# Kernel tuning notes

Measured on AMD Instinct MI355X. Metric: run time of the kernel, lower is better.

The kernel has to match this reference:

```python
import jax, jax.numpy as jnp
import numpy as np

B, T, C, H = 2, 1024, 1024, 16
HD = C // H  # head_dim = 64


def setup_inputs() -> dict:
    key = jax.random.key(0)
    ks = jax.random.split(key, 11)
    s = 0.02  # init scale for weights
    inp = {
        "Q": jax.random.normal(ks[0], (B, T, C), jnp.float32),
        "K": jax.random.normal(ks[1], (B, T, C), jnp.float32),
        "V": jax.random.normal(ks[2], (B, T, C), jnp.float32),
        "Wq": jax.random.normal(ks[3], (C, C), jnp.float32) * s,
        "bq": jnp.zeros((C,), jnp.float32),
        "Wk": jax.random.normal(ks[4], (C, C), jnp.float32) * s,
        "bk": jnp.zeros((C,), jnp.float32),
        "Wv": jax.random.normal(ks[5], (C, C), jnp.float32) * s,
        "bv": jnp.zeros((C,), jnp.float32),
        "Wp": jax.random.normal(ks[6], (C, C), jnp.float32) * s,
        "bp": jax.random.normal(ks[7], (C,), jnp.float32) * s,
        # causal attention mask: True = masked (matches masked_fill semantics)
        "attn_mask": jnp.triu(jnp.ones((T, T), jnp.bool_), k=1),
    }
    return inp


def reference(Q, K, V, Wq, bq, Wk, bk, Wv, bv, Wp, bp, attn_mask):
    b, t, c = Q.shape

    def proj(x, W, bias):
        # nn.Linear: x @ W.T + b, then split heads -> [B, H, T, HD]
        return (x @ W.T + bias).reshape(b, t, H, HD).transpose(0, 2, 1, 3)

    q = proj(Q, Wq, bq)
    k = proj(K, Wk, bk)
    v = proj(V, Wv, bv)
    # scoreF: scaled dot-product -> [B, H, T, T]
    a = jnp.einsum('bhtd,bhsd->bhts', q, k) / jnp.sqrt(jnp.asarray(HD, q.dtype))
    a = jnp.where(attn_mask, -jnp.inf, a)  # masked_fill(attn_mask, -inf)
    a = jax.nn.softmax(a, axis=-1)  # ADropout is identity (p=0)
    y = jnp.einsum('bhts,bhsd->bhtd', a, v)  # a @ v
    y = y.transpose(0, 2, 1, 3).reshape(b, t, c)
    y = y @ Wp.T + bp  # P projection; RDropout identity (p=0)
    return (y, a)
```

## Files before the change

kernel.cpp:

```cpp
#include <hip/hip_runtime.h>
#include <hip/hip_bf16.h>

typedef short bf16x8 __attribute__((ext_vector_type(8)));
typedef float f32x4 __attribute__((ext_vector_type(4)));
typedef unsigned short u16;
typedef u16 u16x8 __attribute__((ext_vector_type(8)));

#define MFMA16(a, b, c) __builtin_amdgcn_mfma_f32_16x16x32_bf16(a, b, c, 0, 0, 0)


__device__ __forceinline__ u16 f2bf(float f) {
    unsigned u = __builtin_bit_cast(unsigned, f);
    unsigned r = (u + 0x7FFFu + ((u >> 16) & 1u)) >> 16;
    return (u16)r;
}

__global__ __launch_bounds__(256) void cvt_bf16(
    const float* __restrict__ Q, const float* __restrict__ K, const float* __restrict__ V,
    const float* __restrict__ Wq, const float* __restrict__ Wk, const float* __restrict__ Wv,
    const float* __restrict__ Wp,
    u16* __restrict__ Qb, u16* __restrict__ Kb, u16* __restrict__ Vb,
    u16* __restrict__ Wqb, u16* __restrict__ Wkb, u16* __restrict__ Wvb,
    u16* __restrict__ Wpb) {
    const int z = blockIdx.y;
    const float* src;
    u16* dst;
    int n;
    switch (z) {
        case 0: src = Q;  dst = Qb;  n = 1 << 21; break;
        case 1: src = K;  dst = Kb;  n = 1 << 21; break;
        case 2: src = V;  dst = Vb;  n = 1 << 21; break;
        case 3: src = Wq; dst = Wqb; n = 1 << 20; break;
        case 4: src = Wk; dst = Wkb; n = 1 << 20; break;
        case 5: src = Wv; dst = Wvb; n = 1 << 20; break;
        default: src = Wp; dst = Wpb; n = 1 << 20; break;
    }
    const int i = (blockIdx.x * 256 + threadIdx.x) * 8;
    if (i >= n) return;
    float4 f0 = *(const float4*)(src + i);
    float4 f1 = *(const float4*)(src + i + 4);
    u16x8 t;
    t[0] = f2bf(f0.x); t[1] = f2bf(f0.y); t[2] = f2bf(f0.z); t[3] = f2bf(f0.w);
    t[4] = f2bf(f1.x); t[5] = f2bf(f1.y); t[6] = f2bf(f1.z); t[7] = f2bf(f1.w);
    *(u16x8*)(dst + i) = t;
}

template <bool OF32>
__device__ inline void gemm_body(const u16* __restrict__ A,
                                 const u16* __restrict__ W,
                                 const float* __restrict__ bias,
                                 void* __restrict__ outp, int mode) {
    __shared__ u16 As[8 * 128 * 8];
    __shared__ u16 Bs[8 * 64 * 8];

    const int tid = threadIdx.x;
    const int wave = tid >> 6, lane = tid & 63;
    const int quad = lane >> 4, l16 = lane & 15;
    const int wm = (wave >> 1) * 64;
    const int wn = (wave & 1) * 32;
    const int m0 = blockIdx.y * 128;
    const int n0 = blockIdx.x * 64;

    f32x4 acc[4][2] = {};

    const int srow = tid >> 3;
    const int sseg = tid & 7;

    for (int kt = 0; kt < 16; ++kt) {
        const int k0 = kt * 64;
        __syncthreads();
#pragma unroll
        for (int rr = 0; rr < 4; ++rr) {
            int row = srow + rr * 32;
            *(uint4*)(As + ((sseg * 128 + row) * 8)) =
                *(const uint4*)(A + (size_t)(m0 + row) * 1024 + k0 + sseg * 8);
        }
#pragma unroll
        for (int rr = 0; rr < 2; ++rr) {
            int row = srow + rr * 32;
            *(uint4*)(Bs + ((sseg * 64 + row) * 8)) =
                *(const uint4*)(W + (size_t)(n0 + row) * 1024 + k0 + sseg * 8);
        }
        __syncthreads();
#pragma unroll
        for (int ks = 0; ks < 2; ++ks) {
            bf16x8 af[4], bfr[2];
#pragma unroll
            for (int mi = 0; mi < 4; ++mi)
                af[mi] = *(const bf16x8*)(As + (((ks * 4 + quad) * 128) + wm + mi * 16 + l16) * 8);
#pragma unroll
            for (int ni = 0; ni < 2; ++ni)
                bfr[ni] = *(const bf16x8*)(Bs + (((ks * 4 + quad) * 64) + wn + ni * 16 + l16) * 8);
#pragma unroll
            for (int mi = 0; mi < 4; ++mi)
#pragma unroll
                for (int ni = 0; ni < 2; ++ni)
                    acc[mi][ni] = MFMA16(af[mi], bfr[ni], acc[mi][ni]);
        }
    }

#pragma unroll
    for (int ni = 0; ni < 2; ++ni) {
        const int n = n0 + wn + ni * 16 + l16;
        const float bv = bias[n];
#pragma unroll
        for (int mi = 0; mi < 4; ++mi) {
#pragma unroll
            for (int r = 0; r < 4; ++r) {
                const int m = m0 + wm + mi * 16 + quad * 4 + r;
                const float val = acc[mi][ni][r] + bv;
                size_t idx;
                if (mode == 0) {
                    int b = m >> 10, t = m & 1023, h = n >> 6, d = n & 63;
                    idx = ((size_t)((b * 16 + h) * 1024 + t)) * 64 + d;
                } else if (mode == 1) {
                    int b = m >> 10, t = m & 1023, h = n >> 6, d = n & 63;
                    idx = ((size_t)((b * 16 + h) * 64 + d)) * 1024 + t;
                } else {
                    idx = (size_t)m * 1024 + n;
                }
                if (OF32) ((float*)outp)[idx] = val;
                else      ((u16*)outp)[idx] = f2bf(val);
            }
        }
    }
}

__global__ __launch_bounds__(256) void proj_qkv(
    const u16* __restrict__ Qb, const u16* __restrict__ Kb, const u16* __restrict__ Vb,
    const u16* __restrict__ Wqb, const u16* __restrict__ Wkb, const u16* __restrict__ Wvb,
    const float* __restrict__ bq, const float* __restrict__ bk, const float* __restrict__ bv,
    u16* __restrict__ q_ws, u16* __restrict__ k_ws, u16* __restrict__ vt_ws) {
    const int z = blockIdx.z;
    const u16* A = (z == 0) ? Qb : (z == 1) ? Kb : Vb;
    const u16* W = (z == 0) ? Wqb : (z == 1) ? Wkb : Wvb;
    const float* bias = (z == 0) ? bq : (z == 1) ? bk : bv;
    u16* out = (z == 0) ? q_ws : (z == 1) ? k_ws : vt_ws;
    gemm_body<false>(A, W, bias, out, (z == 2) ? 1 : 0);
}

__global__ __launch_bounds__(256) void proj_out(
    const u16* __restrict__ A, const u16* __restrict__ Wpb,
    const float* __restrict__ bp, float* __restrict__ y) {
    gemm_body<true>(A, Wpb, bp, y, 2);
}

__global__ __launch_bounds__(256) void attn_fused(
    const u16* __restrict__ q_ws, const u16* __restrict__ k_ws,
    const u16* __restrict__ vt_ws, float* __restrict__ a_out,
    u16* __restrict__ ao_ws) {
    __shared__ u16 P[4][1024];
    __shared__ float Ls[4][16];
    __shared__ float Osum[4][1024];

    const int tid = threadIdx.x;
    const int wave = tid >> 6, lane = tid & 63;
    const int quad = lane >> 4, l16 = lane & 15;
    const int strip = 63 - blockIdx.x;
    const int h = blockIdx.y, b = blockIdx.z;
    const int bh = b * 16 + h;
    const int wrow = strip * 16;
    const int nt = (strip >> 2) + 1;

    const u16* qh = q_ws + (size_t)bh * 65536;
    const u16* kh = k_ws + (size_t)bh * 65536;
    const u16* vh = vt_ws + (size_t)bh * 65536;
    float* ah = a_out + ((size_t)bh << 20);

    bf16x8 qf[2];
    qf[0] = *(const bf16x8*)(qh + (size_t)(wrow + l16) * 64 + quad * 8);
    qf[1] = *(const bf16x8*)(qh + (size_t)(wrow + l16) * 64 + 32 + quad * 8);

    f32x4 c[4][4] = {};
    float sum_r[4] = {0.f, 0.f, 0.f, 0.f};

#pragma unroll
    for (int s = 0; s < 4; ++s) {
        const int ct = wave + s * 4;
        if (ct < nt) {
#pragma unroll
            for (int ks = 0; ks < 2; ++ks)
#pragma unroll
                for (int cb = 0; cb < 4; ++cb) {
                    bf16x8 kf = *(const bf16x8*)(kh + (size_t)(ct * 64 + cb * 16 + l16) * 64 + ks * 32 + quad * 8);
                    c[s][cb] = MFMA16(qf[ks], kf, c[s][cb]);
                }
#pragma unroll
            for (int cb = 0; cb < 4; ++cb) {
                const int col = ct * 64 + cb * 16 + l16;
#pragma unroll
                for (int r = 0; r < 4; ++r) {
                    const int trow = wrow + quad * 4 + r;
                    float E = __expf(c[s][cb][r] * 0.125f - 20.0f);
                    if (col > trow) E = 0.0f;
                    c[s][cb][r] = E;
                    sum_r[r] += E;
                }
            }
        }
    }

    {
        const float4 zz = make_float4(0.f, 0.f, 0.f, 0.f);
        for (int ct = nt + wave; ct < 16; ct += 4) {
#pragma unroll
            for (int j = 0; j < 4; ++j)
                *(float4*)(ah + (size_t)(wrow + j * 4 + quad) * 1024 + ct * 64 + l16 * 4) = zz;
        }
    }

#pragma unroll
    for (int r = 0; r < 4; ++r) {
#pragma unroll
        for (int off = 1; off < 16; off <<= 1)
            sum_r[r] += __shfl_xor(sum_r[r], off);
    }
    if (l16 == 0) {
#pragma unroll
        for (int r = 0; r < 4; ++r) Ls[wave][quad * 4 + r] = sum_r[r];
    }
    __syncthreads();

    float rl[4];
#pragma unroll
    for (int r = 0; r < 4; ++r) {
        const int m = quad * 4 + r;
        rl[r] = 1.0f / (Ls[0][m] + Ls[1][m] + Ls[2][m] + Ls[3][m]);
    }

    f32x4 o[4] = {};
#pragma unroll
    for (int s = 0; s < 4; ++s) {
        const int ct = wave + s * 4;
        if (ct < nt) {
#pragma unroll
            for (int cb = 0; cb < 4; ++cb) {
                const int s_col = cb * 16 + l16;
                const int col = ct * 64 + s_col;
#pragma unroll
                for (int r = 0; r < 4; ++r) {
                    const int m = quad * 4 + r;
                    const float v = c[s][cb][r] * rl[r];
                    ah[(size_t)(wrow + m) * 1024 + col] = v;
                    P[wave][(s_col >> 3) * 128 + m * 8 + (s_col & 7)] = f2bf(v);
                }
            }
#pragma unroll
            for (int ks = 0; ks < 2; ++ks) {
                bf16x8 pf = *(const bf16x8*)(&P[wave][(ks * 4 + quad) * 128 + l16 * 8]);
#pragma unroll
                for (int nb = 0; nb < 4; ++nb) {
                    bf16x8 vf = *(const bf16x8*)(vh + (size_t)(nb * 16 + l16) * 1024 + ct * 64 + ks * 32 + quad * 8);
                    o[nb] = MFMA16(pf, vf, o[nb]);
                }
            }
        }
    }

#pragma unroll
    for (int nb = 0; nb < 4; ++nb)
#pragma unroll
        for (int r = 0; r < 4; ++r) {
            const int row = quad * 4 + r;
            const int d = nb * 16 + l16;
            Osum[wave][row * 64 + (d ^ ((row >> 2) << 4))] = o[nb][r];
        }
    __syncthreads();

#pragma unroll
    for (int i = 0; i < 4; ++i) {
        const int e = tid + i * 256;
        const int row = e >> 6, d = e & 63;
        const int sd = row * 64 + (d ^ ((row >> 2) << 4));
        const float v = Osum[0][sd] + Osum[1][sd] + Osum[2][sd] + Osum[3][sd];
        ao_ws[((size_t)(b * 1024 + wrow + row)) * 1024 + h * 64 + d] = f2bf(v);
    }
}

extern "C" void kernel_launch(void* const* d_in, const int* in_sizes, int n_in,
                              void* d_out, int out_size, void* d_ws, size_t ws_size,
                              hipStream_t stream) {
    const float* Q  = (const float*)d_in[0];
    const float* K  = (const float*)d_in[1];
    const float* V  = (const float*)d_in[2];
    const float* Wq = (const float*)d_in[3];
    const float* bq = (const float*)d_in[4];
    const float* Wk = (const float*)d_in[5];
    const float* bk = (const float*)d_in[6];
    const float* Wv = (const float*)d_in[7];
    const float* bv = (const float*)d_in[8];
    const float* Wp = (const float*)d_in[9];
    const float* bp = (const float*)d_in[10];

    float* y = (float*)d_out;
    float* a = y + (size_t)2 * 1024 * 1024;

    const size_t M1 = (size_t)1 << 20;
    u16* q_ws  = (u16*)d_ws;
    u16* k_ws  = q_ws  + 2 * M1;
    u16* vt_ws = k_ws  + 2 * M1;
    u16* ao_ws = vt_ws + 2 * M1;
    u16* Qb    = ao_ws + 2 * M1;
    u16* Kb    = Qb    + 2 * M1;
    u16* Vb    = Kb    + 2 * M1;
    u16* Wqb   = Vb    + 2 * M1;
    u16* Wkb   = Wqb   + M1;
    u16* Wvb   = Wkb   + M1;
    u16* Wpb   = Wvb   + M1;

    hipLaunchKernelGGL(cvt_bf16, dim3(1024, 7), dim3(256), 0, stream,
                       Q, K, V, Wq, Wk, Wv, Wp, Qb, Kb, Vb, Wqb, Wkb, Wvb, Wpb);
    hipLaunchKernelGGL(proj_qkv, dim3(16, 16, 3), dim3(256), 0, stream,
                       Qb, Kb, Vb, Wqb, Wkb, Wvb, bq, bk, bv, q_ws, k_ws, vt_ws);
    hipLaunchKernelGGL(attn_fused, dim3(64, 16, 2), dim3(256), 0, stream,
                       q_ws, k_ws, vt_ws, a, ao_ws);
    hipLaunchKernelGGL(proj_out, dim3(16, 16, 1), dim3(256), 0, stream,
                       ao_ws, Wpb, bp, y);
}
```

Baseline: 298.4 us.

## Use direct global-to-LDS loads in GEMMs and smaller M tile for output projection

The projection GEMM tile loads now use the global_load_lds builtin, which writes straight into shared memory without passing through registers. The shared-memory tile becomes row-major with 64-element rows instead of the previous k-segment-major layout. The GEMM is templated on the M tile size, and the output projection runs with a 64-row tile on a doubled grid to put more blocks on the GPU. The row-major LDS layout may cause bank conflicts on the MFMA fragment reads, and the GEMMs are small relative to the attention kernel.

```diff
diff --git a/kernel.cpp b/kernel.cpp
--- a/kernel.cpp
+++ b/kernel.cpp
@@ -45,54 +45,58 @@
     *(u16x8*)(dst + i) = t;
 }
 
-template <bool OF32>
+template <int BM, bool OF32>
 __device__ inline void gemm_body(const u16* __restrict__ A,
                                  const u16* __restrict__ W,
                                  const float* __restrict__ bias,
                                  void* __restrict__ outp, int mode) {
-    __shared__ u16 As[8 * 128 * 8];
-    __shared__ u16 Bs[8 * 64 * 8];
+    __shared__ u16 As[BM * 64];
+    __shared__ u16 Bs[64 * 64];
 
     const int tid = threadIdx.x;
     const int wave = tid >> 6, lane = tid & 63;
     const int quad = lane >> 4, l16 = lane & 15;
-    const int wm = (wave >> 1) * 64;
+    constexpr int WM = BM / 2;
+    constexpr int MI = WM / 16;
+    const int wm = (wave >> 1) * WM;
     const int wn = (wave & 1) * 32;
-    const int m0 = blockIdx.y * 128;
+    const int m0 = blockIdx.y * BM;
     const int n0 = blockIdx.x * 64;
 
-    f32x4 acc[4][2] = {};
-
-    const int srow = tid >> 3;
-    const int sseg = tid & 7;
+    f32x4 acc[MI][2] = {};
+
+    const int lrow = lane >> 3;
+    const int lseg = lane & 7;
+    const u16* Ag = A + (size_t)(m0 + wave * 8 + lrow) * 1024 + lseg * 8;
+    const u16* Wg = W + (size_t)(n0 + wave * 8 + lrow) * 1024 + lseg * 8;
+    u16* AsBase = As + wave * 8 * 64;
+    u16* BsBase = Bs + wave * 8 * 64;
 
     for (int kt = 0; kt < 16; ++kt) {
         const int k0 = kt * 64;
         __syncthreads();
 #pragma unroll
-        for (int rr = 0; rr < 4; ++rr) {
-            int row = srow + rr * 32;
-            *(uint4*)(As + ((sseg * 128 + row) * 8)) =
-                *(const uint4*)(A + (size_t)(m0 + row) * 1024 + k0 + sseg * 8);
-        }
-#pragma unroll
-        for (int rr = 0; rr < 2; ++rr) {
-            int row = srow + rr * 32;
-            *(uint4*)(Bs + ((sseg * 64 + row) * 8)) =
-                *(const uint4*)(W + (size_t)(n0 + row) * 1024 + k0 + sseg * 8);
-        }
+        for (int rr = 0; rr < BM / 32; ++rr)
+            __builtin_amdgcn_global_load_lds(
+                (const __attribute__((address_space(1))) void*)(Ag + (size_t)rr * 32 * 1024 + k0),
+                (__attribute__((address_space(3))) void*)(AsBase + rr * 32 * 64), 16, 0, 0);
+#pragma unroll
+        for (int rr = 0; rr < 2; ++rr)
+            __builtin_amdgcn_global_load_lds(
+                (const __attribute__((address_space(1))) void*)(Wg + (size_t)rr * 32 * 1024 + k0),
+                (__attribute__((address_space(3))) void*)(BsBase + rr * 32 * 64), 16, 0, 0);
         __syncthreads();
 #pragma unroll
         for (int ks = 0; ks < 2; ++ks) {
-            bf16x8 af[4], bfr[2];
-#pragma unroll
-            for (int mi = 0; mi < 4; ++mi)
-                af[mi] = *(const bf16x8*)(As + (((ks * 4 + quad) * 128) + wm + mi * 16 + l16) * 8);
+            bf16x8 af[MI], bfr[2];
+#pragma unroll
+            for (int mi = 0; mi < MI; ++mi)
+                af[mi] = *(const bf16x8*)(As + (wm + mi * 16 + l16) * 64 + ks * 32 + quad * 8);
 #pragma unroll
             for (int ni = 0; ni < 2; ++ni)
-                bfr[ni] = *(const bf16x8*)(Bs + (((ks * 4 + quad) * 64) + wn + ni * 16 + l16) * 8);
-#pragma unroll
-            for (int mi = 0; mi < 4; ++mi)
+                bfr[ni] = *(const bf16x8*)(Bs + (wn + ni * 16 + l16) * 64 + ks * 32 + quad * 8);
+#pragma unroll
+            for (int mi = 0; mi < MI; ++mi)
 #pragma unroll
                 for (int ni = 0; ni < 2; ++ni)
                     acc[mi][ni] = MFMA16(af[mi], bfr[ni], acc[mi][ni]);
@@ -104,7 +108,7 @@
         const int n = n0 + wn + ni * 16 + l16;
         const float bv = bias[n];
 #pragma unroll
-        for (int mi = 0; mi < 4; ++mi) {
+        for (int mi = 0; mi < MI; ++mi) {
 #pragma unroll
             for (int r = 0; r < 4; ++r) {
                 const int m = m0 + wm + mi * 16 + quad * 4 + r;
@@ -136,13 +140,13 @@
     const u16* W = (z == 0) ? Wqb : (z == 1) ? Wkb : Wvb;
     const float* bias = (z == 0) ? bq : (z == 1) ? bk : bv;
     u16* out = (z == 0) ? q_ws : (z == 1) ? k_ws : vt_ws;
-    gemm_body<false>(A, W, bias, out, (z == 2) ? 1 : 0);
+    gemm_body<128, false>(A, W, bias, out, (z == 2) ? 1 : 0);
 }
 
 __global__ __launch_bounds__(256) void proj_out(
     const u16* __restrict__ A, const u16* __restrict__ Wpb,
     const float* __restrict__ bp, float* __restrict__ y) {
-    gemm_body<true>(A, Wpb, bp, y, 2);
+    gemm_body<64, true>(A, Wpb, bp, y, 2);
 }
 
 __global__ __launch_bounds__(256) void attn_fused(
@@ -314,6 +318,6 @@
                        Qb, Kb, Vb, Wqb, Wkb, Wvb, bq, bk, bv, q_ws, k_ws, vt_ws);
     hipLaunchKernelGGL(attn_fused, dim3(64, 16, 2), dim3(256), 0, stream,
                        q_ws, k_ws, vt_ws, a, ao_ws);
-    hipLaunchKernelGGL(proj_out, dim3(16, 16, 1), dim3(256), 0, stream,
+    hipLaunchKernelGGL(proj_out, dim3(16, 32, 1), dim3(256), 0, stream,
                        ao_ws, Wpb, bp, y);
 }
```

Measured after the change: 271.8 us. 8.9% less time.
